# Performance work log

Measured on AMD Instinct MI355X. Metric: run time of the kernel, lower is better.

Reference implementation:

```python
import jax, jax.numpy as jnp
import numpy as np

B, C, H, W = 8, 64, 128, 128
O, KS, STRIDE, PAD = 64, 3, 1, 1
K = KS * KS


def setup_inputs() -> dict:
    key = jax.random.key(0)
    k1, k2, k3 = jax.random.split(key, 3)
    x = jax.random.normal(k1, (B, C, H, W), dtype=jnp.float32)
    offset = jax.random.normal(k2, (B, 2 * K, H, W), dtype=jnp.float32)
    weight = jax.random.normal(k3, (O, C, KS, KS), dtype=jnp.float32)
    bias = jnp.zeros((O,), dtype=jnp.float32)
    return {"x": x, "offset": offset, "weight": weight, "bias": bias}


def _deform_conv(x, offset, weight, bias, ks=KS, stride=STRIDE, pad=PAD):
    Bx, Cx, Hx, Wx = x.shape
    Kk = ks * ks
    Ho = (Hx + 2 * pad - ks) // stride + 1
    Wo = (Wx + 2 * pad - ks) // stride + 1
    x_pad = jnp.pad(x, ((0, 0), (0, 0), (pad, pad), (pad, pad)))
    Hp, Wp = Hx + 2 * pad, Wx + 2 * pad
    # base grid (top-left tap, padded coords) -- matches torch code exactly
    ys = jnp.arange(Ho, dtype=x.dtype) * stride
    xs = jnp.arange(Wo, dtype=x.dtype) * stride
    off = offset.reshape(Bx, Kk, 2, Ho, Wo).astype(x.dtype)
    gx = off[:, :, 0] + xs[None, None, None, :]   # [B,K,Ho,Wo]
    gy = off[:, :, 1] + ys[None, None, :, None]
    # bilinear sample with zeros padding (grid_sample align_corners=True round-trips
    # normalization exactly, so we sample at (gy,gx) directly)
    x0 = jnp.floor(gx); y0 = jnp.floor(gy)
    wx1 = gx - x0; wx0 = 1.0 - wx1
    wy1 = gy - y0; wy0 = 1.0 - wy1
    x_flat = x_pad.reshape(Bx, Cx, Hp * Wp)

    def gather(yi, xi, w):
        valid = (xi >= 0) & (xi <= Wp - 1) & (yi >= 0) & (yi <= Hp - 1)
        xi_c = jnp.clip(xi, 0, Wp - 1).astype(jnp.int32)
        yi_c = jnp.clip(yi, 0, Hp - 1).astype(jnp.int32)
        idx = (yi_c * Wp + xi_c).reshape(Bx, -1)           # [B, K*Ho*Wo]
        g = jnp.take_along_axis(x_flat, idx[:, None, :], axis=2)  # [B,C,K*Ho*Wo]
        wv = (w * valid.astype(x.dtype)).reshape(Bx, 1, -1)
        return g * wv

    acc = (gather(y0, x0, wy0 * wx0)
           + gather(y0, x0 + 1.0, wy0 * wx1)
           + gather(y0 + 1.0, x0, wy1 * wx0)
           + gather(y0 + 1.0, x0 + 1.0, wy1 * wx1))
    # channel layout after torch.cat over k: index = k*C + c (k-major)
    sampled = acc.reshape(Bx, Cx, Kk, Ho, Wo).transpose(0, 2, 1, 3, 4)
    sampled = sampled.reshape(Bx, Kk * Cx, Ho, Wo)
    # torch flattens weight as (c, kh, kw) -> index = c*K + k; faithful mismatch
    w_flat = weight.reshape(weight.shape[0], -1).astype(sampled.dtype)  # [O, C*K]
    out = jnp.einsum('oi,bihw->bohw', w_flat, sampled)
    return out + bias[None, :, None, None]


def reference(x, offset, weight, bias):
    return _deform_conv(x, offset, weight, bias)
```

## Files before the change

kernel.cpp:

```cpp
#include <hip/hip_runtime.h>
#include <hip/hip_bf16.h>

#define BB 8
#define CC 64
#define OO 64
#define HH 128
#define WWI 128
#define HWSZ (HH * WWI)
#define KK 9
#define II (KK * CC)

#define PXW 16
#define PYH 8
#define WNX 24
#define WNY 16
#define WROWS (WNX * WNY)

typedef __attribute__((ext_vector_type(8))) short bf16x8;
typedef __attribute__((ext_vector_type(4))) float f32x4;
typedef __attribute__((ext_vector_type(4))) unsigned int uint4v;

__device__ __forceinline__ int iclamp(int v, int lo, int hi) {
    return v < lo ? lo : (v > hi ? hi : v);
}
__device__ __forceinline__ unsigned short f2bf(float f) {
    unsigned u = __float_as_uint(f);
    return (unsigned short)((u + 0x7fffu + ((u >> 16) & 1u)) >> 16);
}
__device__ __forceinline__ float bfl(unsigned u) { return __uint_as_float(u << 16); }
__device__ __forceinline__ float bfh(unsigned u) { return __uint_as_float(u & 0xffff0000u); }

__global__ __launch_bounds__(256) void prep_xt(const float* __restrict__ x,
                                               unsigned short* __restrict__ xt) {
    __shared__ float tile[64][65];
    const int blk = blockIdx.x;
    const int b = blk & 7;
    const int p0 = (blk >> 3) * 64;
    const int t = threadIdx.x;
    const int a = t >> 6;
    const int q = t & 63;
    const float* xb = x + (size_t)b * CC * HWSZ + p0;
#pragma unroll
    for (int r = 0; r < 16; ++r) {
        int c = r * 4 + a;
        tile[c][q] = xb[(size_t)c * HWSZ + q];
    }
    __syncthreads();
    unsigned short* xo = xt + ((size_t)b * HWSZ + p0) * CC;
#pragma unroll
    for (int r = 0; r < 16; ++r) {
        int pl = r * 4 + a;
        xo[(size_t)pl * CC + q] = f2bf(tile[q][pl]);
    }
}

__global__ void prep_waf(const float* __restrict__ w, unsigned short* __restrict__ waf) {
    int tid = blockIdx.x * 256 + threadIdx.x;
    if (tid < 72 * 512) {
        int slab = tid >> 9;
        int r = tid & 511;
        int l = r >> 3, j = r & 7;
        int m = slab & 3;
        int kc = (slab >> 2) & 1;
        int k = slab >> 3;
        int o = m * 16 + (l & 15);
        int i = k * 64 + kc * 32 + (l >> 4) * 8 + j;
        waf[tid] = f2bf(w[(size_t)o * II + i]);
    }
}

__global__ __launch_bounds__(256, 3) void deform_mfma5(
        const unsigned short* __restrict__ xt,
        const float* __restrict__ off,
        const unsigned short* __restrict__ waf,
        const float* __restrict__ bias,
        float* __restrict__ out) {
    __shared__ unsigned short win[WROWS * CC];

    const int blk = blockIdx.x;
    const int b = blk & 7;
    const int pidx = blk >> 3;
    const int y0 = (pidx >> 3) * PYH;
    const int x0 = (pidx & 7) * PXW;
    const int xleft = x0 - 4, ytop = y0 - 4;

    const int t = threadIdx.x;
    const int wave = t >> 6;
    const int lane = t & 63;
    const int fm = lane & 15;
    const int hi = lane >> 4;
    const int c0s = hi * 8;
    const int c1s = 32 + hi * 8;

    const unsigned short* xtb = xt + (size_t)b * HWSZ * CC;
    const float* offpx = off + (size_t)b * 2 * KK * HWSZ
                             + (size_t)(y0 + wave * 2) * WWI + x0 + fm;

    float oxb[2][2], oyb[2][2];
#pragma unroll
    for (int nt = 0; nt < 2; ++nt) {
        oxb[0][nt] = offpx[(size_t)0 * HWSZ + nt * WWI];
        oyb[0][nt] = offpx[(size_t)1 * HWSZ + nt * WWI];
    }

    {
        const int tch = t & 7;
        const int rb = t >> 3;
#pragma unroll
        for (int sw = 0; sw < 12; ++sw) {
            const int r = sw * 32 + rb;
            const int wy = r / WNX, wx = r - wy * WNX;
            const int cy = ytop + wy, cx = xleft + wx;
            if (((unsigned)cy < (unsigned)HH) && ((unsigned)cx < (unsigned)WWI)) {
                const uint4v v = *(const uint4v*)(xtb + (size_t)(cy * WWI + cx) * CC + tch * 8);
                *(uint4v*)&win[r * CC + ((tch ^ (r & 7)) << 3)] = v;
            }
        }
    }
    __syncthreads();

    f32x4 acc[2][4];
#pragma unroll
    for (int nt = 0; nt < 2; ++nt)
#pragma unroll
        for (int m = 0; m < 4; ++m) acc[nt][m] = (f32x4)(0.0f);

#pragma unroll
    for (int k = 0; k < KK; ++k) {
        const int cur = k & 1, nxt = cur ^ 1;
        if (k + 1 < KK) {
#pragma unroll
            for (int nt = 0; nt < 2; ++nt) {
                oxb[nxt][nt] = offpx[(size_t)(2 * k + 2) * HWSZ + nt * WWI];
                oyb[nxt][nt] = offpx[(size_t)(2 * k + 3) * HWSZ + nt * WWI];
            }
        }
        const unsigned short* wk = waf + (size_t)k * 8 * 512 + lane * 8;
        bf16x8 af[8];
#pragma unroll
        for (int q = 0; q < 8; ++q) af[q] = *(const bf16x8*)(wk + (size_t)q * 512);

#pragma unroll
        for (int nt = 0; nt < 2; ++nt) {
            const float gx = oxb[cur][nt] + (float)(x0 + fm);
            const float gy = oyb[cur][nt] + (float)(y0 + wave * 2 + nt);
            const float fxf = floorf(gx), fyf = floorf(gy);
            const float fx = gx - fxf, fy = gy - fyf;
            const int ux0 = (int)fxf - 1, ux1 = (int)fxf;
            const int uy0 = (int)fyf - 1, uy1 = (int)fyf;
            const float vx0 = ((unsigned)ux0 < (unsigned)WWI) ? 1.0f : 0.0f;
            const float vx1 = ((unsigned)ux1 < (unsigned)WWI) ? 1.0f : 0.0f;
            const float vy0 = ((unsigned)uy0 < (unsigned)HH) ? 1.0f : 0.0f;
            const float vy1 = ((unsigned)uy1 < (unsigned)HH) ? 1.0f : 0.0f;
            const float w00 = (1.0f - fy) * (1.0f - fx) * vy0 * vx0;
            const float w01 = (1.0f - fy) * fx          * vy0 * vx1;
            const float w10 = fy          * (1.0f - fx) * vy1 * vx0;
            const float w11 = fy          * fx          * vy1 * vx1;
            const int cx0 = iclamp(ux0, 0, WWI - 1), cx1 = iclamp(ux1, 0, WWI - 1);
            const int cy0 = iclamp(uy0, 0, HH - 1),  cy1 = iclamp(uy1, 0, HH - 1);

            const bool inw = (cx0 >= xleft) & (cx1 <= xleft + WNX - 1)
                           & (cy0 >= ytop) & (cy1 <= ytop + WNY - 1);
            const int wx0 = iclamp(cx0 - xleft, 0, WNX - 1);
            const int wx1 = iclamp(cx1 - xleft, 0, WNX - 1);
            const int wy0 = iclamp(cy0 - ytop, 0, WNY - 1);
            const int wy1 = iclamp(cy1 - ytop, 0, WNY - 1);
            const int r00 = wy0 * WNX + wx0, r01 = wy0 * WNX + wx1;
            const int r10 = wy1 * WNX + wx0, r11 = wy1 * WNX + wx1;

#define LDSRD(r, kc) (*(const uint4v*)&win[(r) * CC + ((((hi) + ((kc) << 2)) ^ ((r) & 7)) << 3)])
            uint4v A0 = LDSRD(r00, 0), A1 = LDSRD(r00, 1);
            uint4v B0 = LDSRD(r01, 0), B1 = LDSRD(r01, 1);
            uint4v C0 = LDSRD(r10, 0), C1 = LDSRD(r10, 1);
            uint4v D0 = LDSRD(r11, 0), D1 = LDSRD(r11, 1);
#undef LDSRD
            if (!inw) {
                const unsigned short* g00 = xtb + (size_t)(cy0 * WWI + cx0) * CC;
                const unsigned short* g01 = xtb + (size_t)(cy0 * WWI + cx1) * CC;
                const unsigned short* g10 = xtb + (size_t)(cy1 * WWI + cx0) * CC;
                const unsigned short* g11 = xtb + (size_t)(cy1 * WWI + cx1) * CC;
                A0 = *(const uint4v*)(g00 + c0s);  A1 = *(const uint4v*)(g00 + c1s);
                B0 = *(const uint4v*)(g01 + c0s);  B1 = *(const uint4v*)(g01 + c1s);
                C0 = *(const uint4v*)(g10 + c0s);  C1 = *(const uint4v*)(g10 + c1s);
                D0 = *(const uint4v*)(g11 + c0s);  D1 = *(const uint4v*)(g11 + c1s);
            }

            bf16x8 bf0, bf1;
            __hip_bfloat162* rp0 = (__hip_bfloat162*)&bf0;
            __hip_bfloat162* rp1 = (__hip_bfloat162*)&bf1;
#pragma unroll
            for (int i = 0; i < 4; ++i) {
                float vlo = w00 * bfl(A0[i]) + w01 * bfl(B0[i])
                          + w10 * bfl(C0[i]) + w11 * bfl(D0[i]);
                float vhi = w00 * bfh(A0[i]) + w01 * bfh(B0[i])
                          + w10 * bfh(C0[i]) + w11 * bfh(D0[i]);
                rp0[i] = __hip_bfloat162{__float2bfloat16(vlo), __float2bfloat16(vhi)};
                float ulo = w00 * bfl(A1[i]) + w01 * bfl(B1[i])
                          + w10 * bfl(C1[i]) + w11 * bfl(D1[i]);
                float uhi = w00 * bfh(A1[i]) + w01 * bfh(B1[i])
                          + w10 * bfh(C1[i]) + w11 * bfh(D1[i]);
                rp1[i] = __hip_bfloat162{__float2bfloat16(ulo), __float2bfloat16(uhi)};
            }
#pragma unroll
            for (int m = 0; m < 4; ++m)
                acc[nt][m] = __builtin_amdgcn_mfma_f32_16x16x32_bf16(af[m], bf0, acc[nt][m], 0, 0, 0);
#pragma unroll
            for (int m = 0; m < 4; ++m)
                acc[nt][m] = __builtin_amdgcn_mfma_f32_16x16x32_bf16(af[4 + m], bf1, acc[nt][m], 0, 0, 0);
        }
    }

#pragma unroll
    for (int nt = 0; nt < 2; ++nt) {
        float* outb = out + (size_t)b * OO * HWSZ
                          + (size_t)(y0 + wave * 2 + nt) * WWI + x0 + fm;
#pragma unroll
        for (int m = 0; m < 4; ++m) {
            const int ob = m * 16 + hi * 4;
            const float4 bs = *(const float4*)(bias + ob);
#pragma unroll
            for (int j = 0; j < 4; ++j) {
                outb[(size_t)(ob + j) * HWSZ] = acc[nt][m][j] + ((const float*)&bs)[j];
            }
        }
    }
}

__global__ __launch_bounds__(256) void deform_conv_fallback(
        const float* __restrict__ x, const float* __restrict__ off,
        const float* __restrict__ wmat, const float* __restrict__ bias,
        float* __restrict__ out) {
    const int b = blockIdx.y;
    const int p = blockIdx.x * 256 + threadIdx.x;
    const int wo = p & (WWI - 1);
    const int ho = p >> 7;
    const float* xb = x + (size_t)b * CC * HWSZ;
    const float* offb = off + (size_t)b * 2 * KK * HWSZ + p;
    float acc[OO];
#pragma unroll
    for (int o = 0; o < OO; ++o) acc[o] = 0.0f;
#pragma unroll 1
    for (int k = 0; k < KK; ++k) {
        const float gx = offb[(size_t)(2 * k + 0) * HWSZ] + (float)wo;
        const float gy = offb[(size_t)(2 * k + 1) * HWSZ] + (float)ho;
        const float fxf = floorf(gx), fyf = floorf(gy);
        const float fx = gx - fxf, fy = gy - fyf;
        const int ux0 = (int)fxf - 1, ux1 = (int)fxf;
        const int uy0 = (int)fyf - 1, uy1 = (int)fyf;
        const float vx0 = ((unsigned)ux0 < (unsigned)WWI) ? 1.0f : 0.0f;
        const float vx1 = ((unsigned)ux1 < (unsigned)WWI) ? 1.0f : 0.0f;
        const float vy0 = ((unsigned)uy0 < (unsigned)HH) ? 1.0f : 0.0f;
        const float vy1 = ((unsigned)uy1 < (unsigned)HH) ? 1.0f : 0.0f;
        const float w00 = (1.0f - fy) * (1.0f - fx) * vy0 * vx0;
        const float w01 = (1.0f - fy) * fx * vy0 * vx1;
        const float w10 = fy * (1.0f - fx) * vy1 * vx0;
        const float w11 = fy * fx * vy1 * vx1;
        const int cx0 = iclamp(ux0, 0, WWI - 1), cx1 = iclamp(ux1, 0, WWI - 1);
        const int cy0 = iclamp(uy0, 0, HH - 1), cy1 = iclamp(uy1, 0, HH - 1);
        const int i00 = cy0 * WWI + cx0, i01 = cy0 * WWI + cx1;
        const int i10 = cy1 * WWI + cx0, i11 = cy1 * WWI + cx1;
#pragma unroll 4
        for (int c = 0; c < CC; ++c) {
            const float* xc = xb + (size_t)c * HWSZ;
            const float v = w00 * xc[i00] + w01 * xc[i01] + w10 * xc[i10] + w11 * xc[i11];
            const float* wrow = wmat + (size_t)(k * CC + c);
#pragma unroll
            for (int o = 0; o < OO; ++o) acc[o] = fmaf(wrow[(size_t)o * II], v, acc[o]);
        }
    }
    float* outb = out + (size_t)b * OO * HWSZ + p;
#pragma unroll
    for (int o = 0; o < OO; ++o) outb[(size_t)o * HWSZ] = acc[o] + bias[o];
}

extern "C" void kernel_launch(void* const* d_in, const int* in_sizes, int n_in,
                              void* d_out, int out_size, void* d_ws, size_t ws_size,
                              hipStream_t stream) {
    const float* x    = (const float*)d_in[0];
    const float* off  = (const float*)d_in[1];
    const float* w    = (const float*)d_in[2];
    const float* bias = (const float*)d_in[3];
    float* out = (float*)d_out;

    const size_t xt_bytes  = (size_t)BB * HWSZ * CC * sizeof(unsigned short);
    const size_t waf_bytes = (size_t)72 * 512 * sizeof(unsigned short);

    if (ws_size >= xt_bytes + waf_bytes) {
        unsigned short* xt  = (unsigned short*)d_ws;
        unsigned short* wfp = (unsigned short*)((char*)d_ws + xt_bytes);
        prep_xt<<<dim3((HWSZ / 64) * BB), 256, 0, stream>>>(x, xt);
        prep_waf<<<(72 * 512 + 255) / 256, 256, 0, stream>>>(w, wfp);
        deform_mfma5<<<dim3(BB * (HH / PYH) * (WWI / PXW)), 256, 0, stream>>>(
            xt, off, wfp, bias, out);
    } else {
        deform_conv_fallback<<<dim3(HWSZ / 256, BB), 256, 0, stream>>>(x, off, w, bias, out);
    }
}
```

Before: 54.88 us.

## Double pixel tile height with 512-thread blocks and packed-float bilinear blend

After: 55.69 us. About the same (+1.5%).

```diff
diff --git a/kernel.cpp b/kernel.cpp
--- a/kernel.cpp
+++ b/kernel.cpp
@@ -11,13 +11,14 @@
 #define II (KK * CC)
 
 #define PXW 16
-#define PYH 8
+#define PYH 16
 #define WNX 24
-#define WNY 16
+#define WNY 24
 #define WROWS (WNX * WNY)
 
 typedef __attribute__((ext_vector_type(8))) short bf16x8;
 typedef __attribute__((ext_vector_type(4))) float f32x4;
+typedef __attribute__((ext_vector_type(2))) float f32x2;
 typedef __attribute__((ext_vector_type(4))) unsigned int uint4v;
 
 __device__ __forceinline__ int iclamp(int v, int lo, int hi) {
@@ -27,8 +28,12 @@
     unsigned u = __float_as_uint(f);
     return (unsigned short)((u + 0x7fffu + ((u >> 16) & 1u)) >> 16);
 }
-__device__ __forceinline__ float bfl(unsigned u) { return __uint_as_float(u << 16); }
-__device__ __forceinline__ float bfh(unsigned u) { return __uint_as_float(u & 0xffff0000u); }
+__device__ __forceinline__ f32x2 unpk(unsigned u) {
+    f32x2 r;
+    r.x = __uint_as_float(u << 16);
+    r.y = __uint_as_float(u & 0xffff0000u);
+    return r;
+}
 
 __global__ __launch_bounds__(256) void prep_xt(const float* __restrict__ x,
                                                unsigned short* __restrict__ xt) {
@@ -69,13 +74,13 @@
     }
 }
 
-__global__ __launch_bounds__(256, 3) void deform_mfma5(
+__global__ __launch_bounds__(512, 3) void deform_mfma6(
         const unsigned short* __restrict__ xt,
         const float* __restrict__ off,
         const unsigned short* __restrict__ waf,
         const float* __restrict__ bias,
         float* __restrict__ out) {
-    __shared__ unsigned short win[WROWS * CC];
+    extern __shared__ unsigned short win[];
 
     const int blk = blockIdx.x;
     const int b = blk & 7;
@@ -107,8 +112,8 @@
         const int tch = t & 7;
         const int rb = t >> 3;
 #pragma unroll
-        for (int sw = 0; sw < 12; ++sw) {
-            const int r = sw * 32 + rb;
+        for (int sw = 0; sw < 9; ++sw) {
+            const int r = sw * 64 + rb;
             const int wy = r / WNX, wx = r - wy * WNX;
             const int cy = ytop + wy, cx = xleft + wx;
             if (((unsigned)cy < (unsigned)HH) && ((unsigned)cx < (unsigned)WWI)) {
@@ -185,21 +190,23 @@
                 D0 = *(const uint4v*)(g11 + c0s);  D1 = *(const uint4v*)(g11 + c1s);
             }
 
+            const f32x2 w00v = {w00, w00}, w01v = {w01, w01};
+            const f32x2 w10v = {w10, w10}, w11v = {w11, w11};
             bf16x8 bf0, bf1;
             __hip_bfloat162* rp0 = (__hip_bfloat162*)&bf0;
             __hip_bfloat162* rp1 = (__hip_bfloat162*)&bf1;
 #pragma unroll
             for (int i = 0; i < 4; ++i) {
-                float vlo = w00 * bfl(A0[i]) + w01 * bfl(B0[i])
-                          + w10 * bfl(C0[i]) + w11 * bfl(D0[i]);
-                float vhi = w00 * bfh(A0[i]) + w01 * bfh(B0[i])
-                          + w10 * bfh(C0[i]) + w11 * bfh(D0[i]);
-                rp0[i] = __hip_bfloat162{__float2bfloat16(vlo), __float2bfloat16(vhi)};
-                float ulo = w00 * bfl(A1[i]) + w01 * bfl(B1[i])
-                          + w10 * bfl(C1[i]) + w11 * bfl(D1[i]);
-                float uhi = w00 * bfh(A1[i]) + w01 * bfh(B1[i])
-                          + w10 * bfh(C1[i]) + w11 * bfh(D1[i]);
-                rp1[i] = __hip_bfloat162{__float2bfloat16(ulo), __float2bfloat16(uhi)};
+                f32x2 r0 = unpk(A0[i]) * w00v;
+                r0 += unpk(B0[i]) * w01v;
+                r0 += unpk(C0[i]) * w10v;
+                r0 += unpk(D0[i]) * w11v;
+                rp0[i] = __hip_bfloat162{__float2bfloat16(r0.x), __float2bfloat16(r0.y)};
+                f32x2 r1 = unpk(A1[i]) * w00v;
+                r1 += unpk(B1[i]) * w01v;
+                r1 += unpk(C1[i]) * w10v;
+                r1 += unpk(D1[i]) * w11v;
+                rp1[i] = __hip_bfloat162{__float2bfloat16(r1.x), __float2bfloat16(r1.y)};
             }
 #pragma unroll
             for (int m = 0; m < 4; ++m)
@@ -290,7 +297,8 @@
         unsigned short* wfp = (unsigned short*)((char*)d_ws + xt_bytes);
         prep_xt<<<dim3((HWSZ / 64) * BB), 256, 0, stream>>>(x, xt);
         prep_waf<<<(72 * 512 + 255) / 256, 256, 0, stream>>>(w, wfp);
-        deform_mfma5<<<dim3(BB * (HH / PYH) * (WWI / PXW)), 256, 0, stream>>>(
+        deform_mfma6<<<dim3(BB * (HH / PYH) * (WWI / PXW)), dim3(512),
+                       WROWS * CC * sizeof(unsigned short), stream>>>(
             xt, off, wfp, bias, out);
     } else {
         deform_conv_fallback<<<dim3(HWSZ / 256, BB), 256, 0, stream>>>(x, off, w, bias, out);
```
